# Kernel tuning notes

Hardware: AMD Instinct MI355X
Metric: run time of the kernel (lower is better)

## Reference

```python
import jax, jax.numpy as jnp
import numpy as np

B, L, H, E = 32, 256, 8, 16
SEQ_LEN = 64          # init seq_len, used only in final view
OUT = 256             # out_channels, must be divisible by SEQ_LEN
A = E + 1 + 128       # augmented channels: original + time + conv(128)
SIG_CH = A + A * A    # depth-2 signature channels
DN = ('NWC', 'WIO', 'NWC')


def setup_inputs() -> dict:
    key = jax.random.key(0)
    ks = jax.random.split(key, 8)
    return {
        'q': jax.random.normal(ks[0], (B, L, H, E), jnp.float32),
        'k': jax.random.normal(ks[1], (B, L, H, E), jnp.float32),
        'v': jax.random.normal(ks[2], (B, L, H, E), jnp.float32),
        'mask': jnp.zeros((B, L), jnp.bool_),
        'conv1_w': jax.random.normal(ks[3], (3, E, 64), jnp.float32) * 0.1,
        'conv1_b': jnp.zeros((64,), jnp.float32),
        'conv2_w': jax.random.normal(ks[4], (1, 64, 128), jnp.float32) * 0.1,
        'conv2_b': jnp.zeros((128,), jnp.float32),
        'lin_w': jax.random.normal(ks[5], (SIG_CH, OUT), jnp.float32) * 0.01,
        'lin_b': jnp.zeros((OUT,), jnp.float32),
    }


def _signature_depth2(p):
    # p: [N, S, C] piecewise-linear path. Returns [N, C + C*C].
    dx = p[:, 1:] - p[:, :-1]                       # [N, S-1, C]
    s1 = dx.sum(axis=1)                             # level 1
    cum_excl = jnp.cumsum(dx, axis=1) - dx          # sum of increments before t
    # level 2: sum_{s<t} dx_s (x) dx_t + 0.5 * dx_t (x) dx_t
    s2 = jnp.einsum('nti,ntj->nij', cum_excl + 0.5 * dx, dx)
    return jnp.concatenate([s1, s2.reshape(s2.shape[0], -1)], axis=-1)


def reference(q, k, v, mask, conv1_w, conv1_b, conv2_w, conv2_b, lin_w, lin_b):
    Bq, Lq, Hq, Eq = q.shape
    x = q.transpose(0, 2, 1, 3).reshape(Bq * Hq, Lq, Eq)   # [N, L, E]
    T = Lq - 3 + 1                                          # valid-conv length, kernel 3
    # Augment pieces
    trunc = x[:, 2:]                                        # [N, T, E]
    time = jnp.broadcast_to(jnp.linspace(0.0, 1.0, T, dtype=x.dtype)[None, :, None],
                            (Bq * Hq, T, 1))
    a = jax.lax.conv_general_dilated(x, conv1_w, (1,), 'VALID', dimension_numbers=DN) + conv1_b
    a = jax.nn.relu(jax.lax.conv_general_dilated(a, conv2_w, (1,), 'VALID', dimension_numbers=DN) + conv2_b)
    aug = jnp.concatenate([trunc, time, a], axis=2)         # [N, T, A]
    # lead-lag transform as written in source: interleave along time -> [N, 2T, A]
    lag = jnp.concatenate([aug[:, 1:], aug[:, -1:]], axis=1)
    ll = jnp.stack([aug, lag], axis=2).reshape(aug.shape[0], 2 * T, aug.shape[2])
    sig = _signature_depth2(ll)                             # [N, SIG_CH]
    out = sig @ lin_w + lin_b                               # [N, OUT]
    return out.reshape(Bq, Hq, SEQ_LEN, -1)
```

## Files before the change

### kernel.cpp

```cpp
#include <hip/hip_runtime.h>
#include <hip/hip_bf16.h>

#define Bq 32
#define Lq 256
#define Hq 8
#define Eq 16
#define Nn (Bq*Hq)
#define T 254
#define A 145
#define SIG_CH (A + A*A)
#define KP 21184
#define OUT 256
#define TPAD 256
#define OTS2 36
#define XAS 72

typedef __attribute__((ext_vector_type(8))) short short8;
typedef __attribute__((ext_vector_type(8))) unsigned short ushort8;
typedef __attribute__((ext_vector_type(4))) float floatx4;

static __device__ __forceinline__ unsigned short f2bf(float v) {
    unsigned int u = __float_as_uint(v);
    unsigned int r = (u + 0x7FFFu + ((u >> 16) & 1u)) >> 16;
    return (unsigned short)r;
}
static __device__ __forceinline__ float bf2f(unsigned short b) {
    return __uint_as_float(((unsigned int)b) << 16);
}

__global__ __launch_bounds__(256) void wsplit_kernel(
    const float* __restrict__ w1, const float* __restrict__ w2,
    unsigned short* __restrict__ w1im_hi, unsigned short* __restrict__ w1im_lo,
    unsigned short* __restrict__ w2t_hi,  unsigned short* __restrict__ w2t_lo)
{
    int idx = blockIdx.x*256 + threadIdx.x;
    if (idx < 4096) {
        int c = idx & 63, k = idx >> 6;
        float v = (k < 48) ? w1[k*64 + c] : 0.f;
        unsigned short hb = f2bf(v);
        w1im_hi[c*64 + k] = hb;
        w1im_lo[c*64 + k] = f2bf(v - bf2f(hb));
    } else {
        int j = idx - 4096;
        int c = j & 127, i = j >> 7;
        float v = w2[i*128 + c];
        unsigned short hb = f2bf(v);
        w2t_hi[c*64 + i] = hb;
        w2t_lo[c*64 + i] = f2bf(v - bf2f(hb));
    }
}

__global__ __launch_bounds__(256) void aug_kernel(
    const float* __restrict__ q,
    const float* __restrict__ b1, const float* __restrict__ b2,
    const unsigned short* __restrict__ w1im_hi, const unsigned short* __restrict__ w1im_lo,
    const unsigned short* __restrict__ w2t_hi,  const unsigned short* __restrict__ w2t_lo,
    float* __restrict__ aug_t)
{
    __shared__ __align__(16) float xs[68*16];
    __shared__ __align__(16) float b1s[64];
    __shared__ __align__(16) float b2s[128];
    __shared__ __align__(16) unsigned short ximh[32*XAS];
    __shared__ __align__(16) unsigned short ximl[32*XAS];
    __shared__ __align__(16) unsigned short a1h[32*XAS];
    __shared__ __align__(16) unsigned short a1l[32*XAS];
    __shared__ __align__(16) float outs[A*OTS2];

    const int tid = threadIdx.x;
    const int n = blockIdx.y;
    const int b = n >> 3, h = n & 7;
    const int tb0 = blockIdx.x * 64;

    const int lane = tid & 63;
    const int wv   = tid >> 6;
    const int frow = lane & 15;
    const int quad = lane >> 4;

    if (tid < 64)  b1s[tid] = b1[tid];
    if (tid < 128) b2s[tid] = b2[tid];
    {
        const float4* q4 = (const float4*)q + ((long)(b*Lq)*Hq + h)*4;
        float4* xs4 = (float4*)xs;
        for (int i = tid; i < 68*4; i += 256) {
            int rr = i >> 2, e4 = i & 3;
            int t = tb0 + rr; if (t > 255) t = 255;
            xs4[rr*4 + e4] = q4[t*32 + e4];
        }
    }
    __syncthreads();

    const float inv253 = 1.0f / 253.0f;

    #pragma unroll 1
    for (int sub = 0; sub < 2; ++sub) {
        const int t0 = tb0 + sub*32;
        const int l0 = sub*32;

        {
            const int tl = tid >> 3, g = tid & 7;
            if (g < 6) {
                const float* src = &xs[(l0 + tl)*16 + g*8];
                float4 v0 = *(const float4*)src;
                float4 v1 = *(const float4*)(src + 4);
                unsigned short hh[8], ll[8];
                #pragma unroll
                for (int e = 0; e < 4; ++e) {
                    float va = (&v0.x)[e], vb = (&v1.x)[e];
                    unsigned short ha = f2bf(va), hb2 = f2bf(vb);
                    hh[e] = ha;     ll[e] = f2bf(va - bf2f(ha));
                    hh[4+e] = hb2;  ll[4+e] = f2bf(vb - bf2f(hb2));
                }
                *(ushort8*)&ximh[tl*XAS + g*8] = *(ushort8*)hh;
                *(ushort8*)&ximl[tl*XAS + g*8] = *(ushort8*)ll;
            } else {
                const ushort8 z8 = {0,0,0,0,0,0,0,0};
                *(ushort8*)&ximh[tl*XAS + g*8] = z8;
                *(ushort8*)&ximl[tl*XAS + g*8] = z8;
            }
        }
        __syncthreads();

        {
            short8 ah[2][2], al[2][2];
            #pragma unroll
            for (int mt = 0; mt < 2; ++mt)
                #pragma unroll
                for (int ks = 0; ks < 2; ++ks) {
                    int ar = (mt*16 + frow)*XAS + ks*32 + quad*8;
                    ah[mt][ks] = *(const short8*)&ximh[ar];
                    al[mt][ks] = *(const short8*)&ximl[ar];
                }
            short8 bh[2], bl[2];
            #pragma unroll
            for (int ks = 0; ks < 2; ++ks) {
                int br = (wv*16 + frow)*64 + ks*32 + quad*8;
                bh[ks] = *(const short8*)(w1im_hi + br);
                bl[ks] = *(const short8*)(w1im_lo + br);
            }
            floatx4 acc1[2];
            acc1[0] = (floatx4){0.f,0.f,0.f,0.f};
            acc1[1] = (floatx4){0.f,0.f,0.f,0.f};
            #pragma unroll
            for (int mt = 0; mt < 2; ++mt)
                #pragma unroll
                for (int ks = 0; ks < 2; ++ks) {
                    acc1[mt] = __builtin_amdgcn_mfma_f32_16x16x32_bf16(ah[mt][ks], bh[ks], acc1[mt], 0,0,0);
                    acc1[mt] = __builtin_amdgcn_mfma_f32_16x16x32_bf16(ah[mt][ks], bl[ks], acc1[mt], 0,0,0);
                    acc1[mt] = __builtin_amdgcn_mfma_f32_16x16x32_bf16(al[mt][ks], bh[ks], acc1[mt], 0,0,0);
                }
            const int c = wv*16 + frow;
            const float bias = b1s[c];
            #pragma unroll
            for (int mt = 0; mt < 2; ++mt)
                #pragma unroll
                for (int e = 0; e < 4; ++e) {
                    int t = mt*16 + quad*4 + e;
                    float v = acc1[mt][e] + bias;
                    unsigned short hb = f2bf(v);
                    a1h[t*XAS + c] = hb;
                    a1l[t*XAS + c] = f2bf(v - bf2f(hb));
                }
        }
        __syncthreads();

        {
            short8 ah[2][2], al[2][2];
            #pragma unroll
            for (int mt = 0; mt < 2; ++mt)
                #pragma unroll
                for (int ks = 0; ks < 2; ++ks) {
                    int ar = (mt*16 + frow)*XAS + ks*32 + quad*8;
                    ah[mt][ks] = *(const short8*)&a1h[ar];
                    al[mt][ks] = *(const short8*)&a1l[ar];
                }
            short8 bh[2][2], bl[2][2];
            #pragma unroll
            for (int nt = 0; nt < 2; ++nt)
                #pragma unroll
                for (int ks = 0; ks < 2; ++ks) {
                    int br = (wv*32 + nt*16 + frow)*64 + ks*32 + quad*8;
                    bh[nt][ks] = *(const short8*)(w2t_hi + br);
                    bl[nt][ks] = *(const short8*)(w2t_lo + br);
                }
            floatx4 acc2[2][2];
            #pragma unroll
            for (int mt = 0; mt < 2; ++mt)
                #pragma unroll
                for (int nt = 0; nt < 2; ++nt)
                    acc2[mt][nt] = (floatx4){0.f,0.f,0.f,0.f};
            #pragma unroll
            for (int mt = 0; mt < 2; ++mt)
                #pragma unroll
                for (int nt = 0; nt < 2; ++nt)
                    #pragma unroll
                    for (int ks = 0; ks < 2; ++ks) {
                        acc2[mt][nt] = __builtin_amdgcn_mfma_f32_16x16x32_bf16(ah[mt][ks], bh[nt][ks], acc2[mt][nt], 0,0,0);
                        acc2[mt][nt] = __builtin_amdgcn_mfma_f32_16x16x32_bf16(ah[mt][ks], bl[nt][ks], acc2[mt][nt], 0,0,0);
                        acc2[mt][nt] = __builtin_amdgcn_mfma_f32_16x16x32_bf16(al[mt][ks], bh[nt][ks], acc2[mt][nt], 0,0,0);
                    }
            #pragma unroll
            for (int mt = 0; mt < 2; ++mt)
                #pragma unroll
                for (int nt = 0; nt < 2; ++nt) {
                    int c = wv*32 + nt*16 + frow;
                    float bias = b2s[c];
                    float4 vv;
                    vv.x = fmaxf(acc2[mt][nt][0] + bias, 0.f);
                    vv.y = fmaxf(acc2[mt][nt][1] + bias, 0.f);
                    vv.z = fmaxf(acc2[mt][nt][2] + bias, 0.f);
                    vv.w = fmaxf(acc2[mt][nt][3] + bias, 0.f);
                    *(float4*)&outs[(17 + c)*OTS2 + mt*16 + quad*4] = vv;
                }
        }

        for (int idx = tid; idx < 17*32; idx += 256) {
            int ch = idx >> 5, tt = idx & 31;
            int t = t0 + tt;
            float val = (ch < 16) ? xs[(l0 + tt + 2)*16 + ch] : (float)t * inv253;
            outs[ch*OTS2 + tt] = val;
        }
        __syncthreads();

        {
            const long nb = (long)n*A;
            for (int idx = tid; idx < A*32; idx += 256) {
                int row = idx >> 5, tt = idx & 31;
                aug_t[(nb + row)*TPAD + t0 + tt] = outs[row*OTS2 + tt];
            }
        }
        __syncthreads();
    }
}

#define CHT 160
#define LDA2 40

__global__ __launch_bounds__(256) void sig_kernel(
    const float* __restrict__ aug_t,
    unsigned short* __restrict__ sig_hi, unsigned short* __restrict__ sig_lo)
{
    __shared__ __align__(16) unsigned short MhT[CHT*LDA2];
    __shared__ __align__(16) unsigned short MlT[CHT*LDA2];
    __shared__ __align__(16) unsigned short DhT[CHT*LDA2];
    __shared__ __align__(16) unsigned short DlT[CHT*LDA2];

    const int tid = threadIdx.x;
    const int n = blockIdx.x;
    const float* an = aug_t + (long)n*A*TPAD;

    const int lane = tid & 63;
    const int w    = tid >> 6;
    const int wm   = w & 1;
    const int wn   = w >> 1;
    const int frow = lane & 15;
    const int quad = lane >> 4;

    const int ch = tid;
    float a0 = 0.f;
    if (ch < A) a0 = an[(long)ch*TPAD];

    floatx4 acc[5][5];
    #pragma unroll
    for (int i = 0; i < 5; ++i)
        #pragma unroll
        for (int j = 0; j < 5; ++j)
            acc[i][j] = (floatx4){0.f, 0.f, 0.f, 0.f};

    for (int c = 0; c < 8; ++c) {
        const int t0 = c*32;
        if (ch < CHT) {
            unsigned short mh[32], ml[32], dh[32], dl[32];
            if (ch < A) {
                float v[33];
                const float* src = an + (long)ch*TPAD + t0;
                #pragma unroll
                for (int i = 0; i < 8; ++i)
                    *(float4*)&v[i*4] = *(const float4*)(src + i*4);
                v[32] = (t0 + 32 <= 253) ? src[32] : 0.f;
                #pragma unroll
                for (int tl = 0; tl < 32; ++tl) {
                    bool valid = (t0 + tl) <= 252;
                    float x0 = v[tl], x1 = v[tl+1];
                    float d = valid ? (x1 - x0) : 0.f;
                    float m = valid ? (0.5f*(x0 + x1) - a0) : 0.f;
                    unsigned short hb = f2bf(m);
                    mh[tl] = hb; ml[tl] = f2bf(m - bf2f(hb));
                    unsigned short db2 = f2bf(d);
                    dh[tl] = db2; dl[tl] = f2bf(d - bf2f(db2));
                }
            } else {
                #pragma unroll
                for (int tl = 0; tl < 32; ++tl) { mh[tl]=0; ml[tl]=0; dh[tl]=0; dl[tl]=0; }
            }
            #pragma unroll
            for (int p = 0; p < 4; ++p) {
                *(ushort8*)&MhT[ch*LDA2 + p*8] = *(ushort8*)&mh[p*8];
                *(ushort8*)&MlT[ch*LDA2 + p*8] = *(ushort8*)&ml[p*8];
                *(ushort8*)&DhT[ch*LDA2 + p*8] = *(ushort8*)&dh[p*8];
                *(ushort8*)&DlT[ch*LDA2 + p*8] = *(ushort8*)&dl[p*8];
            }
        }
        __syncthreads();

        short8 afh[5], afl[5], bfh[5], bfl[5];
        #pragma unroll
        for (int i = 0; i < 5; ++i) {
            int ar = (wm*80 + i*16 + frow)*LDA2 + quad*8;
            int br = (wn*80 + i*16 + frow)*LDA2 + quad*8;
            afh[i] = *(const short8*)&MhT[ar];
            afl[i] = *(const short8*)&MlT[ar];
            bfh[i] = *(const short8*)&DhT[br];
            bfl[i] = *(const short8*)&DlT[br];
        }
        #pragma unroll
        for (int mt = 0; mt < 5; ++mt)
            #pragma unroll
            for (int nt = 0; nt < 5; ++nt) {
                acc[mt][nt] = __builtin_amdgcn_mfma_f32_16x16x32_bf16(
                    afh[mt], bfh[nt], acc[mt][nt], 0, 0, 0);
                acc[mt][nt] = __builtin_amdgcn_mfma_f32_16x16x32_bf16(
                    afh[mt], bfl[nt], acc[mt][nt], 0, 0, 0);
                acc[mt][nt] = __builtin_amdgcn_mfma_f32_16x16x32_bf16(
                    afl[mt], bfh[nt], acc[mt][nt], 0, 0, 0);
            }
        __syncthreads();
    }

    unsigned short* sh = sig_hi + (long)n*KP;
    unsigned short* sl = sig_lo + (long)n*KP;
    if (tid < A) {
        float v = an[(long)tid*TPAD + 253] - a0;
        unsigned short hb = f2bf(v);
        sh[tid] = hb;
        sl[tid] = f2bf(v - bf2f(hb));
    }
    if (tid >= 160 && tid < 160 + (KP - SIG_CH)) {
        sh[SIG_CH + tid - 160] = 0;
        sl[SIG_CH + tid - 160] = 0;
    }
    #pragma unroll
    for (int mt = 0; mt < 5; ++mt)
        #pragma unroll
        for (int nt = 0; nt < 5; ++nt) {
            int j = wn*80 + nt*16 + frow;
            int ib = wm*80 + mt*16 + quad*4;
            #pragma unroll
            for (int e = 0; e < 4; ++e) {
                int i = ib + e;
                if (i < A && j < A) {
                    float v = acc[mt][nt][e];
                    unsigned short hb = f2bf(v);
                    sh[A + i*A + j] = hb;
                    sl[A + i*A + j] = f2bf(v - bf2f(hb));
                }
            }
        }
}

__global__ __launch_bounds__(256) void wconv_kernel(
    const float* __restrict__ W,
    unsigned short* __restrict__ wt_hi, unsigned short* __restrict__ wt_lo)
{
    __shared__ float ls[64][65];
    const int tid = threadIdx.x;
    const int k0 = blockIdx.x * 64;
    const int o0 = blockIdx.y * 64;

    #pragma unroll
    for (int p = 0; p < 16; ++p) {
        int idx = tid + p*256;
        int kk = idx >> 6, oo = idx & 63;
        int k = k0 + kk;
        ls[kk][oo] = (k < SIG_CH) ? W[(long)k*OUT + o0 + oo] : 0.f;
    }
    __syncthreads();

    const int oo = tid >> 2;
    const int kq = (tid & 3) * 16;
    unsigned short hbuf[16], lbuf[16];
    #pragma unroll
    for (int j = 0; j < 16; ++j) {
        float v = ls[kq + j][oo];
        unsigned short hb = f2bf(v);
        hbuf[j] = hb;
        lbuf[j] = f2bf(v - bf2f(hb));
    }
    long off = (long)(o0 + oo)*KP + k0 + kq;
    *(ushort8*)(wt_hi + off)     = *(ushort8*)&hbuf[0];
    *(ushort8*)(wt_hi + off + 8) = *(ushort8*)&hbuf[8];
    *(ushort8*)(wt_lo + off)     = *(ushort8*)&lbuf[0];
    *(ushort8*)(wt_lo + off + 8) = *(ushort8*)&lbuf[8];
}

#define SPLITK 61
#define KC 352
#define NSTEP (KC/32)
#define LDA 40

__global__ __launch_bounds__(256) void gemm_kernel(
    const unsigned short* __restrict__ sig_hi, const unsigned short* __restrict__ sig_lo,
    const unsigned short* __restrict__ wt_hi,  const unsigned short* __restrict__ wt_lo,
    float* __restrict__ part)
{
    __shared__ __align__(16) unsigned short Ah[128*LDA];
    __shared__ __align__(16) unsigned short Al[128*LDA];
    __shared__ __align__(16) unsigned short Bh[128*LDA];
    __shared__ __align__(16) unsigned short Bl[128*LDA];

    const int tid = threadIdx.x;
    const int o0 = blockIdx.x * 128;
    const int n0 = blockIdx.y * 128;
    const int z  = blockIdx.z;
    const int k0 = z * KC;

    const int lane = tid & 63;
    const int w    = tid >> 6;
    const int wm   = w & 1;
    const int wn   = w >> 1;
    const int frow = lane & 15;
    const int quad = lane >> 4;

    const int srow = tid >> 1;
    const int kh   = (tid & 1) * 16;

    const unsigned short* gAh = sig_hi + (long)(n0 + srow)*KP;
    const unsigned short* gAl = sig_lo + (long)(n0 + srow)*KP;
    const unsigned short* gBh = wt_hi  + (long)(o0 + srow)*KP;
    const unsigned short* gBl = wt_lo  + (long)(o0 + srow)*KP;

    ushort8 rah[2], ral[2], rbh[2], rbl[2];
    const ushort8 z8 = {0,0,0,0,0,0,0,0};

    #define GLOAD(s)                                                          \
        {                                                                     \
            int kb = k0 + (s)*32 + kh;                                        \
            if (kb < KP) {                                                    \
                rah[0] = *(const ushort8*)(gAh + kb);                         \
                rah[1] = *(const ushort8*)(gAh + kb + 8);                     \
                ral[0] = *(const ushort8*)(gAl + kb);                         \
                ral[1] = *(const ushort8*)(gAl + kb + 8);                     \
                rbh[0] = *(const ushort8*)(gBh + kb);                         \
                rbh[1] = *(const ushort8*)(gBh + kb + 8);                     \
                rbl[0] = *(const ushort8*)(gBl + kb);                         \
                rbl[1] = *(const ushort8*)(gBl + kb + 8);                     \
            } else {                                                          \
                rah[0]=z8; rah[1]=z8; ral[0]=z8; ral[1]=z8;                   \
                rbh[0]=z8; rbh[1]=z8; rbl[0]=z8; rbl[1]=z8;                   \
            }                                                                 \
        }

    #define LSTORE()                                                          \
        {                                                                     \
            int o = srow*LDA + kh;                                            \
            *(ushort8*)(Ah + o)     = rah[0];                                 \
            *(ushort8*)(Ah + o + 8) = rah[1];                                 \
            *(ushort8*)(Al + o)     = ral[0];                                 \
            *(ushort8*)(Al + o + 8) = ral[1];                                 \
            *(ushort8*)(Bh + o)     = rbh[0];                                 \
            *(ushort8*)(Bh + o + 8) = rbh[1];                                 \
            *(ushort8*)(Bl + o)     = rbl[0];                                 \
            *(ushort8*)(Bl + o + 8) = rbl[1];                                 \
        }

    floatx4 acc[4][4];
    #pragma unroll
    for (int i = 0; i < 4; ++i)
        #pragma unroll
        for (int j = 0; j < 4; ++j)
            acc[i][j] = (floatx4){0.f, 0.f, 0.f, 0.f};

    GLOAD(0);
    LSTORE();
    __syncthreads();

    for (int s = 0; s < NSTEP; ++s) {
        if (s < NSTEP-1) GLOAD(s+1);

        short8 afh[4], afl[4], bfh[4], bfl[4];
        const int aoff = (wm*64 + frow)*LDA + quad*8;
        const int boff = (wn*64 + frow)*LDA + quad*8;
        #pragma unroll
        for (int tI = 0; tI < 4; ++tI) {
            afh[tI] = *(const short8*)(Ah + aoff + tI*16*LDA);
            afl[tI] = *(const short8*)(Al + aoff + tI*16*LDA);
            bfh[tI] = *(const short8*)(Bh + boff + tI*16*LDA);
            bfl[tI] = *(const short8*)(Bl + boff + tI*16*LDA);
        }
        #pragma unroll
        for (int mt = 0; mt < 4; ++mt)
            #pragma unroll
            for (int nt = 0; nt < 4; ++nt) {
                acc[mt][nt] = __builtin_amdgcn_mfma_f32_16x16x32_bf16(
                    afh[mt], bfh[nt], acc[mt][nt], 0, 0, 0);
                acc[mt][nt] = __builtin_amdgcn_mfma_f32_16x16x32_bf16(
                    afh[mt], bfl[nt], acc[mt][nt], 0, 0, 0);
                acc[mt][nt] = __builtin_amdgcn_mfma_f32_16x16x32_bf16(
                    afl[mt], bfh[nt], acc[mt][nt], 0, 0, 0);
            }
        __syncthreads();
        if (s < NSTEP-1) {
            LSTORE();
            __syncthreads();
        }
    }

    float* pz = part + (long)z * (Nn*OUT);
    #pragma unroll
    for (int mt = 0; mt < 4; ++mt)
        #pragma unroll
        for (int nt = 0; nt < 4; ++nt) {
            int col = o0 + wn*64 + nt*16 + frow;
            int rbase = n0 + wm*64 + mt*16 + quad*4;
            #pragma unroll
            for (int e = 0; e < 4; ++e)
                pz[(long)(rbase + e)*OUT + col] = acc[mt][nt][e];
        }
}

__global__ __launch_bounds__(256) void reduce_kernel(
    const float* __restrict__ part, const float* __restrict__ lb,
    float* __restrict__ out)
{
    int idx = blockIdx.x * 256 + threadIdx.x;
    float s = lb[idx & 255];
    #pragma unroll 8
    for (int z = 0; z < SPLITK; ++z)
        s += part[(long)z * (Nn*OUT) + idx];
    out[idx] = s;
}

extern "C" void kernel_launch(void* const* d_in, const int* in_sizes, int n_in,
                              void* d_out, int out_size, void* d_ws, size_t ws_size,
                              hipStream_t stream) {
    const float* q  = (const float*)d_in[0];
    const float* w1 = (const float*)d_in[4];
    const float* b1 = (const float*)d_in[5];
    const float* w2 = (const float*)d_in[6];
    const float* b2 = (const float*)d_in[7];
    const float* lw = (const float*)d_in[8];
    const float* lb = (const float*)d_in[9];
    float* out = (float*)d_out;

    char* ws = (char*)d_ws;
    unsigned short* w1im_hi = (unsigned short*)ws;
    unsigned short* w1im_lo = (unsigned short*)(ws + 8192);
    unsigned short* w2t_hi  = (unsigned short*)(ws + 16384);
    unsigned short* w2t_lo  = (unsigned short*)(ws + 32768);
    unsigned short* sig_hi  = (unsigned short*)ws;
    unsigned short* sig_lo  = (unsigned short*)(ws + 10846208);
    float*          aug_t   = (float*)(ws + 21692416);
    unsigned short* wt_hi   = (unsigned short*)(ws + 21692416);
    unsigned short* wt_lo   = (unsigned short*)(ws + 32538624);
    float*          part    = (float*)(ws + 43384832);

    wsplit_kernel<<<48, 256, 0, stream>>>(w1, w2, w1im_hi, w1im_lo, w2t_hi, w2t_lo);
    aug_kernel<<<dim3(4, Nn), 256, 0, stream>>>(q, b1, b2, w1im_hi, w1im_lo, w2t_hi, w2t_lo, aug_t);
    sig_kernel<<<Nn, 256, 0, stream>>>(aug_t, sig_hi, sig_lo);
    wconv_kernel<<<dim3(KP/64, OUT/64), 256, 0, stream>>>(lw, wt_hi, wt_lo);
    gemm_kernel<<<dim3(2, 2, SPLITK), 256, 0, stream>>>(sig_hi, sig_lo, wt_hi, wt_lo, part);
    reduce_kernel<<<(Nn*OUT)/256, 256, 0, stream>>>(part, lb, out);
}
```

Baseline: 181.1 us.

## Fuse augmentation convs into signature kernel and drop low-part of increments

```diff
diff --git a/kernel.cpp b/kernel.cpp
--- a/kernel.cpp
+++ b/kernel.cpp
@@ -11,9 +11,6 @@
 #define SIG_CH (A + A*A)
 #define KP 21184
 #define OUT 256
-#define TPAD 256
-#define OTS2 36
-#define XAS 72
 
 typedef __attribute__((ext_vector_type(8))) short short8;
 typedef __attribute__((ext_vector_type(8))) unsigned short ushort8;
@@ -50,83 +47,94 @@
     }
 }
 
-__global__ __launch_bounds__(256) void aug_kernel(
+#define MDS 40
+#define OS3 36
+#define XIS 72
+
+__global__ __launch_bounds__(256) void augsig_kernel(
     const float* __restrict__ q,
     const float* __restrict__ b1, const float* __restrict__ b2,
     const unsigned short* __restrict__ w1im_hi, const unsigned short* __restrict__ w1im_lo,
     const unsigned short* __restrict__ w2t_hi,  const unsigned short* __restrict__ w2t_lo,
-    float* __restrict__ aug_t)
+    unsigned short* __restrict__ sig_hi, unsigned short* __restrict__ sig_lo)
 {
-    __shared__ __align__(16) float xs[68*16];
+    __shared__ __align__(16) unsigned short mdb[3*160*MDS];
+    __shared__ __align__(16) float outs[A*OS3];
+    __shared__ __align__(16) float xsc[36*16];
     __shared__ __align__(16) float b1s[64];
     __shared__ __align__(16) float b2s[128];
-    __shared__ __align__(16) unsigned short ximh[32*XAS];
-    __shared__ __align__(16) unsigned short ximl[32*XAS];
-    __shared__ __align__(16) unsigned short a1h[32*XAS];
-    __shared__ __align__(16) unsigned short a1l[32*XAS];
-    __shared__ __align__(16) float outs[A*OTS2];
+
+    unsigned short* Mh = mdb;
+    unsigned short* Ml = mdb + 160*MDS;
+    unsigned short* Dh = mdb + 2*160*MDS;
+    unsigned short* ximh = mdb;
+    unsigned short* ximl = mdb + 3456;
+    unsigned short* a1h  = mdb + 6912;
+    unsigned short* a1l  = mdb + 10368;
 
     const int tid = threadIdx.x;
-    const int n = blockIdx.y;
+    const int n = blockIdx.x;
     const int b = n >> 3, h = n & 7;
-    const int tb0 = blockIdx.x * 64;
 
     const int lane = tid & 63;
     const int wv   = tid >> 6;
     const int frow = lane & 15;
     const int quad = lane >> 4;
+    const int wm = wv & 1, wn = wv >> 1;
 
     if (tid < 64)  b1s[tid] = b1[tid];
     if (tid < 128) b2s[tid] = b2[tid];
-    {
-        const float4* q4 = (const float4*)q + ((long)(b*Lq)*Hq + h)*4;
-        float4* xs4 = (float4*)xs;
-        for (int i = tid; i < 68*4; i += 256) {
-            int rr = i >> 2, e4 = i & 3;
-            int t = tb0 + rr; if (t > 255) t = 255;
-            xs4[rr*4 + e4] = q4[t*32 + e4];
-        }
-    }
-    __syncthreads();
-
+
+    const float4* q4 = (const float4*)q + ((long)(b*Lq)*Hq + h)*4;
     const float inv253 = 1.0f / 253.0f;
 
+    float a0 = 0.f, vlast = 0.f;
+
+    floatx4 acc[5][5];
+    #pragma unroll
+    for (int i = 0; i < 5; ++i)
+        #pragma unroll
+        for (int j = 0; j < 5; ++j)
+            acc[i][j] = (floatx4){0.f, 0.f, 0.f, 0.f};
+
     #pragma unroll 1
-    for (int sub = 0; sub < 2; ++sub) {
-        const int t0 = tb0 + sub*32;
-        const int l0 = sub*32;
+    for (int c = 0; c < 8; ++c) {
+        const int t0 = c*32;
+
+        if (tid < 140) {
+            int r = tid >> 2, e4 = tid & 3;
+            int t = t0 + r; if (t > 255) t = 255;
+            *((float4*)xsc + (r*4 + e4)) = q4[t*32 + e4];
+        }
+        __syncthreads();
+
+        for (int idx = tid; idx < 48*8; idx += 256) {
+            int r = idx >> 3, g = idx & 7;
+            unsigned short hh[8], ll[8];
+            if (r <= 32 && g < 6) {
+                const float* src = &xsc[r*16 + g*8];
+                #pragma unroll
+                for (int e = 0; e < 8; ++e) {
+                    float v = src[e];
+                    unsigned short hb = f2bf(v);
+                    hh[e] = hb; ll[e] = f2bf(v - bf2f(hb));
+                }
+            } else {
+                #pragma unroll
+                for (int e = 0; e < 8; ++e) { hh[e] = 0; ll[e] = 0; }
+            }
+            *(ushort8*)&ximh[r*XIS + g*8] = *(ushort8*)hh;
+            *(ushort8*)&ximl[r*XIS + g*8] = *(ushort8*)ll;
+        }
+        __syncthreads();
 
         {
-            const int tl = tid >> 3, g = tid & 7;
-            if (g < 6) {
-                const float* src = &xs[(l0 + tl)*16 + g*8];
-                float4 v0 = *(const float4*)src;
-                float4 v1 = *(const float4*)(src + 4);
-                unsigned short hh[8], ll[8];
-                #pragma unroll
-                for (int e = 0; e < 4; ++e) {
-                    float va = (&v0.x)[e], vb = (&v1.x)[e];
-                    unsigned short ha = f2bf(va), hb2 = f2bf(vb);
-                    hh[e] = ha;     ll[e] = f2bf(va - bf2f(ha));
-                    hh[4+e] = hb2;  ll[4+e] = f2bf(vb - bf2f(hb2));
-                }
-                *(ushort8*)&ximh[tl*XAS + g*8] = *(ushort8*)hh;
-                *(ushort8*)&ximl[tl*XAS + g*8] = *(ushort8*)ll;
-            } else {
-                const ushort8 z8 = {0,0,0,0,0,0,0,0};
-                *(ushort8*)&ximh[tl*XAS + g*8] = z8;
-                *(ushort8*)&ximl[tl*XAS + g*8] = z8;
-            }
-        }
-        __syncthreads();
-
-        {
-            short8 ah[2][2], al[2][2];
-            #pragma unroll
-            for (int mt = 0; mt < 2; ++mt)
+            short8 ah[3][2], al[3][2];
+            #pragma unroll
+            for (int mt = 0; mt < 3; ++mt)
                 #pragma unroll
                 for (int ks = 0; ks < 2; ++ks) {
-                    int ar = (mt*16 + frow)*XAS + ks*32 + quad*8;
+                    int ar = (mt*16 + frow)*XIS + ks*32 + quad*8;
                     ah[mt][ks] = *(const short8*)&ximh[ar];
                     al[mt][ks] = *(const short8*)&ximl[ar];
                 }
@@ -137,39 +145,39 @@
                 bh[ks] = *(const short8*)(w1im_hi + br);
                 bl[ks] = *(const short8*)(w1im_lo + br);
             }
-            floatx4 acc1[2];
-            acc1[0] = (floatx4){0.f,0.f,0.f,0.f};
-            acc1[1] = (floatx4){0.f,0.f,0.f,0.f};
-            #pragma unroll
-            for (int mt = 0; mt < 2; ++mt)
+            floatx4 acc1[3];
+            #pragma unroll
+            for (int mt = 0; mt < 3; ++mt) acc1[mt] = (floatx4){0.f,0.f,0.f,0.f};
+            #pragma unroll
+            for (int mt = 0; mt < 3; ++mt)
                 #pragma unroll
                 for (int ks = 0; ks < 2; ++ks) {
                     acc1[mt] = __builtin_amdgcn_mfma_f32_16x16x32_bf16(ah[mt][ks], bh[ks], acc1[mt], 0,0,0);
                     acc1[mt] = __builtin_amdgcn_mfma_f32_16x16x32_bf16(ah[mt][ks], bl[ks], acc1[mt], 0,0,0);
                     acc1[mt] = __builtin_amdgcn_mfma_f32_16x16x32_bf16(al[mt][ks], bh[ks], acc1[mt], 0,0,0);
                 }
-            const int c = wv*16 + frow;
-            const float bias = b1s[c];
-            #pragma unroll
-            for (int mt = 0; mt < 2; ++mt)
+            const int cc = wv*16 + frow;
+            const float bias = b1s[cc];
+            #pragma unroll
+            for (int mt = 0; mt < 3; ++mt)
                 #pragma unroll
                 for (int e = 0; e < 4; ++e) {
                     int t = mt*16 + quad*4 + e;
                     float v = acc1[mt][e] + bias;
                     unsigned short hb = f2bf(v);
-                    a1h[t*XAS + c] = hb;
-                    a1l[t*XAS + c] = f2bf(v - bf2f(hb));
+                    a1h[t*XIS + cc] = hb;
+                    a1l[t*XIS + cc] = f2bf(v - bf2f(hb));
                 }
         }
         __syncthreads();
 
         {
-            short8 ah[2][2], al[2][2];
-            #pragma unroll
-            for (int mt = 0; mt < 2; ++mt)
+            short8 ah[3][2], al[3][2];
+            #pragma unroll
+            for (int mt = 0; mt < 3; ++mt)
                 #pragma unroll
                 for (int ks = 0; ks < 2; ++ks) {
-                    int ar = (mt*16 + frow)*XAS + ks*32 + quad*8;
+                    int ar = (mt*16 + frow)*XIS + ks*32 + quad*8;
                     ah[mt][ks] = *(const short8*)&a1h[ar];
                     al[mt][ks] = *(const short8*)&a1l[ar];
                 }
@@ -182,14 +190,14 @@
                     bh[nt][ks] = *(const short8*)(w2t_hi + br);
                     bl[nt][ks] = *(const short8*)(w2t_lo + br);
                 }
-            floatx4 acc2[2][2];
-            #pragma unroll
-            for (int mt = 0; mt < 2; ++mt)
+            floatx4 acc2[3][2];
+            #pragma unroll
+            for (int mt = 0; mt < 3; ++mt)
                 #pragma unroll
                 for (int nt = 0; nt < 2; ++nt)
                     acc2[mt][nt] = (floatx4){0.f,0.f,0.f,0.f};
             #pragma unroll
-            for (int mt = 0; mt < 2; ++mt)
+            for (int mt = 0; mt < 3; ++mt)
                 #pragma unroll
                 for (int nt = 0; nt < 2; ++nt)
                     #pragma unroll
@@ -199,84 +207,39 @@
                         acc2[mt][nt] = __builtin_amdgcn_mfma_f32_16x16x32_bf16(al[mt][ks], bh[nt][ks], acc2[mt][nt], 0,0,0);
                     }
             #pragma unroll
-            for (int mt = 0; mt < 2; ++mt)
+            for (int mt = 0; mt < 3; ++mt)
                 #pragma unroll
                 for (int nt = 0; nt < 2; ++nt) {
-                    int c = wv*32 + nt*16 + frow;
-                    float bias = b2s[c];
-                    float4 vv;
-                    vv.x = fmaxf(acc2[mt][nt][0] + bias, 0.f);
-                    vv.y = fmaxf(acc2[mt][nt][1] + bias, 0.f);
-                    vv.z = fmaxf(acc2[mt][nt][2] + bias, 0.f);
-                    vv.w = fmaxf(acc2[mt][nt][3] + bias, 0.f);
-                    *(float4*)&outs[(17 + c)*OTS2 + mt*16 + quad*4] = vv;
-                }
-        }
-
-        for (int idx = tid; idx < 17*32; idx += 256) {
-            int ch = idx >> 5, tt = idx & 31;
-            int t = t0 + tt;
-            float val = (ch < 16) ? xs[(l0 + tt + 2)*16 + ch] : (float)t * inv253;
-            outs[ch*OTS2 + tt] = val;
+                    int cc = wv*32 + nt*16 + frow;
+                    float bias = b2s[cc];
+                    int tb = mt*16 + quad*4;
+                    if (tb <= 32) {
+                        float4 vv;
+                        vv.x = fmaxf(acc2[mt][nt][0] + bias, 0.f);
+                        vv.y = fmaxf(acc2[mt][nt][1] + bias, 0.f);
+                        vv.z = fmaxf(acc2[mt][nt][2] + bias, 0.f);
+                        vv.w = fmaxf(acc2[mt][nt][3] + bias, 0.f);
+                        *(float4*)&outs[(17 + cc)*OS3 + tb] = vv;
+                    }
+                }
+        }
+        for (int idx = tid; idx < 17*33; idx += 256) {
+            int ch = idx / 33, tt = idx - ch*33;
+            float val = (ch < 16) ? xsc[(tt+2)*16 + ch] : (float)(t0+tt)*inv253;
+            outs[ch*OS3 + tt] = val;
         }
         __syncthreads();
 
-        {
-            const long nb = (long)n*A;
-            for (int idx = tid; idx < A*32; idx += 256) {
-                int row = idx >> 5, tt = idx & 31;
-                aug_t[(nb + row)*TPAD + t0 + tt] = outs[row*OTS2 + tt];
-            }
-        }
-        __syncthreads();
-    }
-}
-
-#define CHT 160
-#define LDA2 40
-
-__global__ __launch_bounds__(256) void sig_kernel(
-    const float* __restrict__ aug_t,
-    unsigned short* __restrict__ sig_hi, unsigned short* __restrict__ sig_lo)
-{
-    __shared__ __align__(16) unsigned short MhT[CHT*LDA2];
-    __shared__ __align__(16) unsigned short MlT[CHT*LDA2];
-    __shared__ __align__(16) unsigned short DhT[CHT*LDA2];
-    __shared__ __align__(16) unsigned short DlT[CHT*LDA2];
-
-    const int tid = threadIdx.x;
-    const int n = blockIdx.x;
-    const float* an = aug_t + (long)n*A*TPAD;
-
-    const int lane = tid & 63;
-    const int w    = tid >> 6;
-    const int wm   = w & 1;
-    const int wn   = w >> 1;
-    const int frow = lane & 15;
-    const int quad = lane >> 4;
-
-    const int ch = tid;
-    float a0 = 0.f;
-    if (ch < A) a0 = an[(long)ch*TPAD];
-
-    floatx4 acc[5][5];
-    #pragma unroll
-    for (int i = 0; i < 5; ++i)
-        #pragma unroll
-        for (int j = 0; j < 5; ++j)
-            acc[i][j] = (floatx4){0.f, 0.f, 0.f, 0.f};
-
-    for (int c = 0; c < 8; ++c) {
-        const int t0 = c*32;
-        if (ch < CHT) {
-            unsigned short mh[32], ml[32], dh[32], dl[32];
-            if (ch < A) {
+        if (tid < 160) {
+            unsigned short mh[32], ml[32], dh[32];
+            if (tid < A) {
                 float v[33];
-                const float* src = an + (long)ch*TPAD + t0;
                 #pragma unroll
                 for (int i = 0; i < 8; ++i)
-                    *(float4*)&v[i*4] = *(const float4*)(src + i*4);
-                v[32] = (t0 + 32 <= 253) ? src[32] : 0.f;
+                    *(float4*)&v[i*4] = *(const float4*)&outs[tid*OS3 + i*4];
+                v[32] = outs[tid*OS3 + 32];
+                if (c == 0) a0 = v[0];
+                if (c == 7) vlast = v[29];
                 #pragma unroll
                 for (int tl = 0; tl < 32; ++tl) {
                     bool valid = (t0 + tl) <= 252;
@@ -285,51 +248,47 @@
                     float m = valid ? (0.5f*(x0 + x1) - a0) : 0.f;
                     unsigned short hb = f2bf(m);
                     mh[tl] = hb; ml[tl] = f2bf(m - bf2f(hb));
-                    unsigned short db2 = f2bf(d);
-                    dh[tl] = db2; dl[tl] = f2bf(d - bf2f(db2));
+                    dh[tl] = f2bf(d);
                 }
             } else {
                 #pragma unroll
-                for (int tl = 0; tl < 32; ++tl) { mh[tl]=0; ml[tl]=0; dh[tl]=0; dl[tl]=0; }
-            }
-            #pragma unroll
-            for (int p = 0; p < 4; ++p) {
-                *(ushort8*)&MhT[ch*LDA2 + p*8] = *(ushort8*)&mh[p*8];
-                *(ushort8*)&MlT[ch*LDA2 + p*8] = *(ushort8*)&ml[p*8];
-                *(ushort8*)&DhT[ch*LDA2 + p*8] = *(ushort8*)&dh[p*8];
-                *(ushort8*)&DlT[ch*LDA2 + p*8] = *(ushort8*)&dl[p*8];
+                for (int tl = 0; tl < 32; ++tl) { mh[tl]=0; ml[tl]=0; dh[tl]=0; }
+            }
+            #pragma unroll
+            for (int pp = 0; pp < 4; ++pp) {
+                *(ushort8*)&Mh[tid*MDS + pp*8] = *(ushort8*)&mh[pp*8];
+                *(ushort8*)&Ml[tid*MDS + pp*8] = *(ushort8*)&ml[pp*8];
+                *(ushort8*)&Dh[tid*MDS + pp*8] = *(ushort8*)&dh[pp*8];
             }
         }
         __syncthreads();
 
-        short8 afh[5], afl[5], bfh[5], bfl[5];
-        #pragma unroll
-        for (int i = 0; i < 5; ++i) {
-            int ar = (wm*80 + i*16 + frow)*LDA2 + quad*8;
-            int br = (wn*80 + i*16 + frow)*LDA2 + quad*8;
-            afh[i] = *(const short8*)&MhT[ar];
-            afl[i] = *(const short8*)&MlT[ar];
-            bfh[i] = *(const short8*)&DhT[br];
-            bfl[i] = *(const short8*)&DlT[br];
-        }
-        #pragma unroll
-        for (int mt = 0; mt < 5; ++mt)
-            #pragma unroll
-            for (int nt = 0; nt < 5; ++nt) {
-                acc[mt][nt] = __builtin_amdgcn_mfma_f32_16x16x32_bf16(
-                    afh[mt], bfh[nt], acc[mt][nt], 0, 0, 0);
-                acc[mt][nt] = __builtin_amdgcn_mfma_f32_16x16x32_bf16(
-                    afh[mt], bfl[nt], acc[mt][nt], 0, 0, 0);
-                acc[mt][nt] = __builtin_amdgcn_mfma_f32_16x16x32_bf16(
-                    afl[mt], bfh[nt], acc[mt][nt], 0, 0, 0);
-            }
-        __syncthreads();
+        {
+            short8 afh[5], afl[5], bfh[5];
+            #pragma unroll
+            for (int i = 0; i < 5; ++i) {
+                int ar = (wm*80 + i*16 + frow)*MDS + quad*8;
+                int br = (wn*80 + i*16 + frow)*MDS + quad*8;
+                afh[i] = *(const short8*)&Mh[ar];
+                afl[i] = *(const short8*)&Ml[ar];
+                bfh[i] = *(const short8*)&Dh[br];
+            }
+            #pragma unroll
+            for (int mt = 0; mt < 5; ++mt)
+                #pragma unroll
+                for (int nt = 0; nt < 5; ++nt) {
+                    acc[mt][nt] = __builtin_amdgcn_mfma_f32_16x16x32_bf16(
+                        afh[mt], bfh[nt], acc[mt][nt], 0, 0, 0);
+                    acc[mt][nt] = __builtin_amdgcn_mfma_f32_16x16x32_bf16(
+                        afl[mt], bfh[nt], acc[mt][nt], 0, 0, 0);
+                }
+        }
     }
 
     unsigned short* sh = sig_hi + (long)n*KP;
     unsigned short* sl = sig_lo + (long)n*KP;
     if (tid < A) {
-        float v = an[(long)tid*TPAD + 253] - a0;
+        float v = vlast - a0;
         unsigned short hb = f2bf(v);
         sh[tid] = hb;
         sl[tid] = f2bf(v - bf2f(hb));
@@ -542,20 +501,18 @@
     float* out = (float*)d_out;
 
     char* ws = (char*)d_ws;
-    unsigned short* w1im_hi = (unsigned short*)ws;
-    unsigned short* w1im_lo = (unsigned short*)(ws + 8192);
-    unsigned short* w2t_hi  = (unsigned short*)(ws + 16384);
-    unsigned short* w2t_lo  = (unsigned short*)(ws + 32768);
     unsigned short* sig_hi  = (unsigned short*)ws;
     unsigned short* sig_lo  = (unsigned short*)(ws + 10846208);
-    float*          aug_t   = (float*)(ws + 21692416);
     unsigned short* wt_hi   = (unsigned short*)(ws + 21692416);
     unsigned short* wt_lo   = (unsigned short*)(ws + 32538624);
     float*          part    = (float*)(ws + 43384832);
+    unsigned short* w1im_hi = (unsigned short*)(ws + 43384832);
+    unsigned short* w1im_lo = (unsigned short*)(ws + 43384832 + 8192);
+    unsigned short* w2t_hi  = (unsigned short*)(ws + 43384832 + 16384);
+    unsigned short* w2t_lo  = (unsigned short*)(ws + 43384832 + 32768);
 
     wsplit_kernel<<<48, 256, 0, stream>>>(w1, w2, w1im_hi, w1im_lo, w2t_hi, w2t_lo);
-    aug_kernel<<<dim3(4, Nn), 256, 0, stream>>>(q, b1, b2, w1im_hi, w1im_lo, w2t_hi, w2t_lo, aug_t);
-    sig_kernel<<<Nn, 256, 0, stream>>>(aug_t, sig_hi, sig_lo);
+    augsig_kernel<<<Nn, 256, 0, stream>>>(q, b1, b2, w1im_hi, w1im_lo, w2t_hi, w2t_lo, sig_hi, sig_lo);
     wconv_kernel<<<dim3(KP/64, OUT/64), 256, 0, stream>>>(lw, wt_hi, wt_lo);
     gemm_kernel<<<dim3(2, 2, SPLITK), 256, 0, stream>>>(sig_hi, sig_lo, wt_hi, wt_lo, part);
     reduce_kernel<<<(Nn*OUT)/256, 256, 0, stream>>>(part, lb, out);
```

Result: faster. 170.9 us (-5.6%).
